# Performance work log

Measured on AMD Instinct MI355X. Metric: run time of the kernel, lower is better.

The kernel has to match this reference:

```python
import jax, jax.numpy as jnp
import numpy as np

B, S, H = 1, 2048, 2048
NH, NKV, HD = 16, 4, 128
E, K, I = 16, 4, 1024
ISH = 1024  # moe_intermediate_size * num_shared_experts
EPS = 1e-6
THETA = 10000.0


def setup_inputs():
    key = jax.random.key(0)
    ks = jax.random.split(key, 8)
    sd = 0.02
    return {
        "hidden_states": jax.random.normal(ks[0], (B, S, H), jnp.float32),
        "position_ids": jnp.broadcast_to(jnp.arange(S, dtype=jnp.int32), (B, S)),
        "ln1_w": jnp.ones((H,), jnp.float32),
        "ln2_w": jnp.ones((H,), jnp.float32),
        "w_qkv": jax.random.normal(ks[1], (H, (NH + 2 * NKV) * HD), jnp.float32) * sd,
        "w_o": jax.random.normal(ks[2], (NH * HD, H), jnp.float32) * sd,
        "w_gate": jax.random.normal(ks[3], (H, E), jnp.float32) * sd,
        "w_gu": jax.random.normal(ks[4], (E, H, 2 * I), jnp.float32) * sd,
        "w_down": jax.random.normal(ks[5], (E, I, H), jnp.float32) * sd,
        "w_sh_gu": jax.random.normal(ks[6], (H, 2 * ISH), jnp.float32) * sd,
        "w_sh_down": jax.random.normal(ks[7], (ISH, H), jnp.float32) * sd,
    }


def rmsnorm(x, w):
    xf = x.astype(jnp.float32)
    var = jnp.mean(xf * xf, axis=-1, keepdims=True)
    return (xf * jax.lax.rsqrt(var + EPS)).astype(x.dtype) * w


def apply_rope(x, pos):
    # x: [B, S, nh, HD]; neox style, rotary_dim == head_dim
    half = HD // 2
    inv_freq = 1.0 / (THETA ** (jnp.arange(0, HD, 2, dtype=jnp.float32) / HD))
    freqs = pos.astype(jnp.float32)[..., None] * inv_freq  # [B,S,half]
    cos = jnp.cos(freqs)[:, :, None, :]
    sin = jnp.sin(freqs)[:, :, None, :]
    x1, x2 = x[..., :half], x[..., half:]
    return jnp.concatenate([x1 * cos - x2 * sin, x1 * sin + x2 * cos], axis=-1)


def reference(hidden_states, position_ids, ln1_w, ln2_w, w_qkv, w_o, w_gate,
              w_gu, w_down, w_sh_gu, w_sh_down):
    # --- input RMSNorm (residual is None on entry) ---
    residual = hidden_states
    x = rmsnorm(hidden_states, ln1_w)

    # --- attention (GQA + neox RoPE, causal) ---
    qkv = x @ w_qkv
    q = qkv[..., : NH * HD].reshape(B, S, NH, HD)
    k = qkv[..., NH * HD:(NH + NKV) * HD].reshape(B, S, NKV, HD)
    v = qkv[..., (NH + NKV) * HD:].reshape(B, S, NKV, HD)
    q = apply_rope(q, position_ids)
    k = apply_rope(k, position_ids)
    rep = NH // NKV
    k = jnp.repeat(k, rep, axis=2)
    v = jnp.repeat(v, rep, axis=2)
    scores = jnp.einsum('bqhd,bkhd->bhqk', q, k) * (HD ** -0.5)
    causal = jnp.tril(jnp.ones((S, S), bool))
    scores = jnp.where(causal[None, None], scores, jnp.float32(-1e9))
    probs = jax.nn.softmax(scores, axis=-1)
    ctx = jnp.einsum('bhqk,bkhd->bqhd', probs, v).reshape(B, S, NH * HD)
    attn_out = ctx @ w_o

    # --- fused add + post-attention RMSNorm ---
    residual = residual + attn_out
    x = rmsnorm(residual, ln2_w)

    # --- MoE ---
    xt = x.reshape(-1, H)  # [T, H]
    logits = xt @ w_gate
    rprobs = jax.nn.softmax(logits, axis=-1)
    tw, ti = jax.lax.top_k(rprobs, K)  # [T,K]
    tw = tw / jnp.sum(tw, axis=-1, keepdims=True)  # norm_topk_prob=True
    combine = jnp.sum(jax.nn.one_hot(ti, E, dtype=tw.dtype) * tw[..., None], axis=1)  # [T,E]

    moe_out = jnp.zeros_like(xt)
    for e in range(E):  # fixed small expert count
        gu = xt @ w_gu[e]
        g, u = jnp.split(gu, 2, axis=-1)
        y = (jax.nn.silu(g) * u) @ w_down[e]
        moe_out = moe_out + combine[:, e:e + 1] * y

    # shared expert MLP
    gu = xt @ w_sh_gu
    g, u = jnp.split(gu, 2, axis=-1)
    moe_out = moe_out + (jax.nn.silu(g) * u) @ w_sh_down

    hidden = residual + moe_out.reshape(B, S, H)
    return hidden
```

## Files before the change

kernel.cpp:

```cpp
#include <hip/hip_runtime.h>
#include <hip/hip_bf16.h>
#include <math.h>

#define DI __device__ __forceinline__

typedef __attribute__((ext_vector_type(8))) short bf16x8;
typedef __attribute__((ext_vector_type(4))) short bf16x4;
typedef __attribute__((ext_vector_type(8))) _Float16 f16x8;
typedef __attribute__((ext_vector_type(4))) _Float16 f16x4;
typedef __attribute__((ext_vector_type(4))) float f32x4;

DI float b2f(short s) {
    unsigned u = ((unsigned)(unsigned short)s) << 16;
    return __builtin_bit_cast(float, u);
}
DI short f2b(float f) {
    unsigned u = __builtin_bit_cast(unsigned, f);
    unsigned r = (u + 0x7fffu + ((u >> 16) & 1u)) >> 16;
    return (short)(unsigned short)r;
}
struct hl16 { _Float16 h, l; };
DI hl16 fsp(float f) {
    hl16 r;
    r.h = (_Float16)f;
    r.l = (_Float16)((f - (float)r.h) * 2048.0f);
    return r;
}

template <int MODE>
__global__ __launch_bounds__(256) void rmsnorm_k(const float* __restrict__ x,
                                                 const float* __restrict__ w,
                                                 void* __restrict__ o1,
                                                 void* __restrict__ o2) {
    int row = blockIdx.x, tid = threadIdx.x;
    const float* xr = x + (long)row * 2048;
    float4 a = *(const float4*)(xr + tid * 8);
    float4 b = *(const float4*)(xr + tid * 8 + 4);
    float ss = a.x * a.x + a.y * a.y + a.z * a.z + a.w * a.w +
               b.x * b.x + b.y * b.y + b.z * b.z + b.w * b.w;
    for (int m = 1; m < 64; m <<= 1) ss += __shfl_xor(ss, m);
    __shared__ float red[4];
    if ((tid & 63) == 0) red[tid >> 6] = ss;
    __syncthreads();
    float sc = rsqrtf((red[0] + red[1] + red[2] + red[3]) * (1.0f / 2048.0f) + 1e-6f);
    float4 wa = *(const float4*)(w + tid * 8);
    float4 wb = *(const float4*)(w + tid * 8 + 4);
    float v[8] = {a.x * sc * wa.x, a.y * sc * wa.y, a.z * sc * wa.z, a.w * sc * wa.w,
                  b.x * sc * wb.x, b.y * sc * wb.y, b.z * sc * wb.z, b.w * sc * wb.w};
    if (MODE == 0) {
        f16x8 h, l;
        for (int j = 0; j < 8; ++j) { hl16 t = fsp(v[j]); h[j] = t.h; l[j] = t.l; }
        *(f16x8*)((_Float16*)o1 + (long)row * 2048 + tid * 8) = h;
        *(f16x8*)((_Float16*)o2 + (long)row * 2048 + tid * 8) = l;
    } else {
        bf16x8 o;
        for (int j = 0; j < 8; ++j) o[j] = f2b(v[j]);
        *(bf16x8*)((short*)o1 + (long)row * 2048 + tid * 8) = o;
    }
}

__global__ __launch_bounds__(256) void tsplit_k(const float* __restrict__ in, int ldin,
                                                _Float16* __restrict__ outh,
                                                _Float16* __restrict__ outl, int ldout) {
    __shared__ float t[64][68];
    int r0 = blockIdx.x * 64, c0 = blockIdx.y * 64;
    int tid = threadIdx.x;
    int rr = tid >> 2, cs = (tid & 3) * 16;
    const float* src = in + (long)(r0 + rr) * ldin + c0 + cs;
    for (int u = 0; u < 4; ++u) {
        float4 v = *(const float4*)(src + u * 4);
        t[rr][cs + u * 4 + 0] = v.x; t[rr][cs + u * 4 + 1] = v.y;
        t[rr][cs + u * 4 + 2] = v.z; t[rr][cs + u * 4 + 3] = v.w;
    }
    __syncthreads();
    int cr = tid >> 2, rs = (tid & 3) * 16;
    f16x8 h0, l0, h1, l1;
    for (int u = 0; u < 8; ++u)  { hl16 e = fsp(t[rs + u][cr]);     h0[u] = e.h; l0[u] = e.l; }
    for (int u = 0; u < 8; ++u)  { hl16 e = fsp(t[rs + 8 + u][cr]); h1[u] = e.h; l1[u] = e.l; }
    long ob = (long)(c0 + cr) * ldout + r0 + rs;
    *(f16x8*)(outh + ob) = h0; *(f16x8*)(outh + ob + 8) = h1;
    *(f16x8*)(outl + ob) = l0; *(f16x8*)(outl + ob + 8) = l1;
}

__global__ __launch_bounds__(256) void wprep_k(const float* __restrict__ in,
                                               short* __restrict__ outp,
                                               int R, int C) {
    __shared__ float t[64][68];
    int r0 = blockIdx.x * 64, c0 = blockIdx.y * 64;
    long es = (long)R * C;
    in += blockIdx.z * es;
    outp += blockIdx.z * es;
    int tid = threadIdx.x;
    int rr = tid >> 2, cs = (tid & 3) * 16;
    const float* src = in + (long)(r0 + rr) * C + c0 + cs;
    for (int u = 0; u < 4; ++u) {
        float4 v = *(const float4*)(src + u * 4);
        t[rr][cs + u * 4 + 0] = v.x; t[rr][cs + u * 4 + 1] = v.y;
        t[rr][cs + u * 4 + 2] = v.z; t[rr][cs + u * 4 + 3] = v.w;
    }
    __syncthreads();
    int cr = tid >> 2, rs = (tid & 3) * 16;
    bf16x8 o0, o1;
    for (int u = 0; u < 8; ++u) o0[u] = f2b(t[rs + u][cr]);
    for (int u = 0; u < 8; ++u) o1[u] = f2b(t[rs + 8 + u][cr]);
    long ob = (long)(c0 + cr) * R + r0 + rs;
    *(bf16x8*)(outp + ob) = o0;
    *(bf16x8*)(outp + ob + 8) = o1;
}

enum { EPI_F32 = 0, EPI_RESID = 1 };

template <int EPI>
__global__ __launch_bounds__(256) void pgemm_k(
    const _Float16* __restrict__ Ah, const _Float16* __restrict__ Al, int lda,
    const _Float16* __restrict__ Bh, const _Float16* __restrict__ Bl, int ldb,
    float* __restrict__ C, int ldc,
    const float* __restrict__ resid, int K) {
    __shared__ __align__(16) _Float16 sAh[128][72], sAl[128][72];
    __shared__ __align__(16) _Float16 sBh[64][72], sBl[64][72];
    int n0 = blockIdx.x * 64, m0 = blockIdx.y * 128;
    int tid = threadIdx.x, lane = tid & 63, wv = tid >> 6;
    int wm = (wv >> 1) * 64, wn = (wv & 1) * 32;
    int ln = lane & 15, g8 = (lane >> 4) * 8, rg = lane >> 4;
    int tr = tid >> 3, tc = (tid & 7) * 8;

    f32x4 a1[4][2], a2[4][2];
    for (int i = 0; i < 4; ++i)
        for (int j = 0; j < 2; ++j) { a1[i][j] = f32x4{0,0,0,0}; a2[i][j] = f32x4{0,0,0,0}; }

    for (int k0 = 0; k0 < K; k0 += 64) {
        for (int s = 0; s < 4; ++s) {
            int r = tr + s * 32;
            long ga = (long)(m0 + r) * lda + k0 + tc;
            *(f16x8*)&sAh[r][tc] = *(const f16x8*)(Ah + ga);
            *(f16x8*)&sAl[r][tc] = *(const f16x8*)(Al + ga);
        }
        for (int s = 0; s < 2; ++s) {
            int r = tr + s * 32;
            long gb = (long)(n0 + r) * ldb + k0 + tc;
            *(f16x8*)&sBh[r][tc] = *(const f16x8*)(Bh + gb);
            *(f16x8*)&sBl[r][tc] = *(const f16x8*)(Bl + gb);
        }
        __syncthreads();
        for (int kk = 0; kk < 2; ++kk) {
            f16x8 ah[4], alo[4], bh[2], blo[2];
            for (int i = 0; i < 4; ++i) {
                int r = wm + i * 16 + ln;
                ah[i]  = *(const f16x8*)&sAh[r][kk * 32 + g8];
                alo[i] = *(const f16x8*)&sAl[r][kk * 32 + g8];
            }
            for (int j = 0; j < 2; ++j) {
                int r = wn + j * 16 + ln;
                bh[j]  = *(const f16x8*)&sBh[r][kk * 32 + g8];
                blo[j] = *(const f16x8*)&sBl[r][kk * 32 + g8];
            }
            for (int i = 0; i < 4; ++i)
                for (int j = 0; j < 2; ++j) {
                    a1[i][j] = __builtin_amdgcn_mfma_f32_16x16x32_f16(ah[i], bh[j], a1[i][j], 0, 0, 0);
                    a2[i][j] = __builtin_amdgcn_mfma_f32_16x16x32_f16(alo[i], bh[j], a2[i][j], 0, 0, 0);
                    a2[i][j] = __builtin_amdgcn_mfma_f32_16x16x32_f16(ah[i], blo[j], a2[i][j], 0, 0, 0);
                }
        }
        __syncthreads();
    }
    for (int i = 0; i < 4; ++i)
        for (int r = 0; r < 4; ++r) {
            int m = m0 + wm + i * 16 + rg * 4 + r;
            for (int j = 0; j < 2; ++j) {
                int col = n0 + wn + j * 16 + ln;
                float v = a1[i][j][r] + a2[i][j][r] * (1.0f / 2048.0f);
                if (EPI == EPI_RESID) v += resid[(long)m * ldc + col];
                C[(long)m * ldc + col] = v;
            }
        }
}

enum { MEPI_BF16 = 0, MEPI_ATOMIC = 1 };

template <int EPI, bool EXPERT>
__global__ __launch_bounds__(256) void bgemm_k(
    const short* __restrict__ A, int lda,
    const short* __restrict__ Bt, int ldb, long bStride,
    void* __restrict__ C, int ldc,
    const int* __restrict__ perm, const float* __restrict__ permw,
    const int* __restrict__ offsets,
    int K, int gatherA, int gatherC) {
    __shared__ __align__(16) short sA[128][72], sB[128][72];

    int n0 = blockIdx.x * 128;
    int base = 0, cnt = 1 << 30, m0;
    if (EXPERT) {
        int e = blockIdx.y >> 4;
        m0 = (blockIdx.y & 15) * 128;
        base = offsets[e];
        cnt = offsets[e + 1] - base;
        if (m0 >= cnt) return;
        Bt += (long)e * bStride;
    } else {
        m0 = blockIdx.y * 128;
    }

    int tid = threadIdx.x, lane = tid & 63, wv = tid >> 6;
    int wm = (wv >> 1) * 64, wn = (wv & 1) * 64;
    int ln = lane & 15, g8 = (lane >> 4) * 8, rg = lane >> 4;
    int tr = tid >> 3, tc = (tid & 7) * 8;

    const short* aRow[4];
    for (int s = 0; s < 4; ++s) {
        int m = m0 + tr + s * 32;
        if (EXPERT && m >= cnt) m = cnt - 1;
        int arow;
        if (EXPERT) arow = gatherA ? perm[base + m] : (base + m);
        else arow = m;
        aRow[s] = A + (long)arow * lda;
    }

    f32x4 acc[4][4];
    for (int i = 0; i < 4; ++i)
        for (int j = 0; j < 4; ++j) acc[i][j] = f32x4{0.f, 0.f, 0.f, 0.f};

    for (int k0 = 0; k0 < K; k0 += 64) {
        for (int s = 0; s < 4; ++s) {
            int r = tr + s * 32;
            *(bf16x8*)&sA[r][tc] = *(const bf16x8*)(aRow[s] + k0 + tc);
            *(bf16x8*)&sB[r][tc] = *(const bf16x8*)(Bt + (long)(n0 + r) * ldb + k0 + tc);
        }
        __syncthreads();
        for (int kk = 0; kk < 2; ++kk) {
            bf16x8 af[4], bfr[4];
            for (int i = 0; i < 4; ++i)
                af[i] = *(const bf16x8*)&sA[wm + i * 16 + ln][kk * 32 + g8];
            for (int j = 0; j < 4; ++j)
                bfr[j] = *(const bf16x8*)&sB[wn + j * 16 + ln][kk * 32 + g8];
            for (int i = 0; i < 4; ++i)
                for (int j = 0; j < 4; ++j)
                    acc[i][j] = __builtin_amdgcn_mfma_f32_16x16x32_bf16(af[i], bfr[j], acc[i][j], 0, 0, 0);
        }
        __syncthreads();
    }

    for (int i = 0; i < 4; ++i) {
        for (int r = 0; r < 4; ++r) {
            int m = m0 + wm + i * 16 + rg * 4 + r;
            if (EXPERT && m >= cnt) continue;
            int crow;
            if (EXPERT) crow = gatherC ? perm[base + m] : (base + m);
            else crow = m;
            float cs = 1.0f;
            if (EPI == MEPI_ATOMIC && EXPERT && gatherC) cs = permw[base + m];
            for (int j = 0; j < 4; ++j) {
                int col = n0 + wn + j * 16 + ln;
                float v = acc[i][j][r];
                if (EPI == MEPI_BF16)
                    ((short*)C)[(long)crow * ldc + col] = f2b(v);
                else
                    atomicAdd(&((float*)C)[(long)crow * ldc + col], v * cs);
            }
        }
    }
}

__global__ __launch_bounds__(64) void ropetab_k(const int* __restrict__ pos,
                                                float* __restrict__ tab) {
    int s = blockIdx.x, d = threadIdx.x;
    double inv = pow(10000.0, -(double)d / 64.0);
    double fr = (double)pos[s] * inv;
    tab[s * 128 + d] = (float)cos(fr);
    tab[s * 128 + 64 + d] = (float)sin(fr);
}

__global__ __launch_bounds__(256) void ropeall_k(float* __restrict__ qkvf,
                                                 const float* __restrict__ tab,
                                                 _Float16* __restrict__ kh,
                                                 _Float16* __restrict__ kl) {
    int s = blockIdx.x, sub = threadIdx.x >> 6, d = threadIdx.x & 63;
    int hh = blockIdx.y * 4 + sub;
    float c = tab[s * 128 + d], sn = tab[s * 128 + 64 + d];
    if (hh < 16) {
        float* row = qkvf + (long)s * 3072 + hh * 128;
        float x1 = row[d], x2 = row[d + 64];
        row[d] = x1 * c - x2 * sn;
        row[d + 64] = x1 * sn + x2 * c;
    } else {
        int kvh = hh - 16;
        const float* row = qkvf + (long)s * 3072 + 2048 + kvh * 128;
        float x1 = row[d], x2 = row[d + 64];
        float y1 = x1 * c - x2 * sn, y2 = x1 * sn + x2 * c;
        hl16 a = fsp(y1), b = fsp(y2);
        long base = ((long)kvh * 2048 + s) * 128;
        kh[base + d] = a.h; kl[base + d] = a.l;
        kh[base + 64 + d] = b.h; kl[base + 64 + d] = b.l;
    }
}

__global__ __launch_bounds__(256) void vprep_k(const float* __restrict__ qkvf,
                                               _Float16* __restrict__ vth,
                                               _Float16* __restrict__ vtl) {
    __shared__ float t[64][68];
    int s0 = blockIdx.x * 64, d0 = blockIdx.y * 64, kvh = blockIdx.z;
    int tid = threadIdx.x;
    int rr = tid >> 2, cs = (tid & 3) * 16;
    const float* src = qkvf + (long)(s0 + rr) * 3072 + 2560 + kvh * 128 + d0 + cs;
    for (int u = 0; u < 4; ++u) {
        float4 v = *(const float4*)(src + u * 4);
        t[rr][cs + u * 4 + 0] = v.x; t[rr][cs + u * 4 + 1] = v.y;
        t[rr][cs + u * 4 + 2] = v.z; t[rr][cs + u * 4 + 3] = v.w;
    }
    __syncthreads();
    int dr = tid >> 2, ss = (tid & 3) * 16;
    f16x8 h0, l0, h1, l1;
    for (int u = 0; u < 8; ++u)  { hl16 e = fsp(t[ss + u][dr]);     h0[u] = e.h; l0[u] = e.l; }
    for (int u = 0; u < 8; ++u)  { hl16 e = fsp(t[ss + 8 + u][dr]); h1[u] = e.h; l1[u] = e.l; }
    long ob = ((long)kvh * 128 + d0 + dr) * 2048 + s0 + ss;
    *(f16x8*)(vth + ob) = h0; *(f16x8*)(vth + ob + 8) = h1;
    *(f16x8*)(vtl + ob) = l0; *(f16x8*)(vtl + ob + 8) = l1;
}

__global__ __launch_bounds__(256) void attn_k(
    const float* __restrict__ qkvf,
    const _Float16* __restrict__ kh, const _Float16* __restrict__ kl,
    const _Float16* __restrict__ vth, const _Float16* __restrict__ vtl,
    float* __restrict__ opart, float* __restrict__ mpart, float* __restrict__ lpart) {
    __shared__ __align__(16) _Float16 sKh[32][136], sKl[32][136];
    __shared__ __align__(16) _Float16 sVh[128][44], sVl[128][44];
    __shared__ __align__(16) _Float16 sPh[4][16][44], sPl[4][16][44];

    int bid = blockIdx.x, h = blockIdx.y, kvh = h >> 2;
    int qt = 0, cum = 0;
    for (int q = 0; q < 32; ++q) {
        int ch = (q >> 2) + 1;
        if (bid < cum + ch) { qt = q; break; }
        cum += ch;
    }
    int ci = bid - cum;
    int nt = 2 * (qt + 1);
    int t0 = ci * 8;
    int t1 = t0 + 8 < nt ? t0 + 8 : nt;
    int q0 = qt * 64;
    int tid = threadIdx.x, lane = tid & 63, wv = tid >> 6;
    int ln = lane & 15, g8 = (lane >> 4) * 8, rg = lane >> 4;

    f16x8 qh[4], ql[4];
    {
        int qrow = q0 + wv * 16 + ln;
        for (int ds = 0; ds < 4; ++ds) {
            const float* qp = qkvf + (long)qrow * 3072 + h * 128 + ds * 32 + g8;
            for (int j = 0; j < 8; ++j) { hl16 t = fsp(qp[j]); qh[ds][j] = t.h; ql[ds][j] = t.l; }
        }
    }

    f32x4 o[8];
    for (int i = 0; i < 8; ++i) o[i] = f32x4{0, 0, 0, 0};
    float mrow[4], lrow[4], al[4];
    for (int r = 0; r < 4; ++r) { mrow[r] = -3e38f; lrow[r] = 0.0f; }
    const float scale = 0.08838834764831845f;
    const float ILO = 1.0f / 2048.0f;

    int kr = tid >> 3, kc = (tid & 7) * 16;
    int vr = tid >> 1, vc = (tid & 1) * 16;

    for (int kt = t0; kt < t1; ++kt) {
        int kb = kt * 32;
        {
            long gb = ((long)kvh * 2048 + kb + kr) * 128 + kc;
            *(f16x8*)&sKh[kr][kc]     = *(const f16x8*)(kh + gb);
            *(f16x8*)&sKh[kr][kc + 8] = *(const f16x8*)(kh + gb + 8);
            *(f16x8*)&sKl[kr][kc]     = *(const f16x8*)(kl + gb);
            *(f16x8*)&sKl[kr][kc + 8] = *(const f16x8*)(kl + gb + 8);
        }
        {
            long gb = ((long)kvh * 128 + vr) * 2048 + kb + vc;
            *(f16x8*)&sVh[vr][vc]     = *(const f16x8*)(vth + gb);
            *(f16x8*)&sVh[vr][vc + 8] = *(const f16x8*)(vth + gb + 8);
            *(f16x8*)&sVl[vr][vc]     = *(const f16x8*)(vtl + gb);
            *(f16x8*)&sVl[vr][vc + 8] = *(const f16x8*)(vtl + gb + 8);
        }
        __syncthreads();

        f32x4 s1[2], s2[2];
        for (int j = 0; j < 2; ++j) { s1[j] = f32x4{0,0,0,0}; s2[j] = f32x4{0,0,0,0}; }
        for (int ds = 0; ds < 4; ++ds)
            for (int j = 0; j < 2; ++j) {
                int r = j * 16 + ln;
                f16x8 kfh = *(const f16x8*)&sKh[r][ds * 32 + g8];
                f16x8 kfl = *(const f16x8*)&sKl[r][ds * 32 + g8];
                s1[j] = __builtin_amdgcn_mfma_f32_16x16x32_f16(qh[ds], kfh, s1[j], 0, 0, 0);
                s2[j] = __builtin_amdgcn_mfma_f32_16x16x32_f16(ql[ds], kfh, s2[j], 0, 0, 0);
                s2[j] = __builtin_amdgcn_mfma_f32_16x16x32_f16(qh[ds], kfl, s2[j], 0, 0, 0);
            }

        float sv[2][4];
        bool dg = (kt >= 2 * qt);
        for (int j = 0; j < 2; ++j)
            for (int r = 0; r < 4; ++r) {
                float v = (s1[j][r] + s2[j][r] * ILO) * scale;
                if (dg) {
                    int col = kb + j * 16 + ln;
                    int rw = q0 + wv * 16 + rg * 4 + r;
                    if (col > rw) v = -1e9f;
                }
                sv[j][r] = v;
            }
        for (int r = 0; r < 4; ++r) {
            float mx = fmaxf(sv[0][r], sv[1][r]);
            for (int m = 1; m < 16; m <<= 1) mx = fmaxf(mx, __shfl_xor(mx, m));
            float mn = fmaxf(mrow[r], mx);
            al[r] = __expf(mrow[r] - mn);
            mrow[r] = mn;
            float rs = 0.0f;
            for (int j = 0; j < 2; ++j) {
                float p = __expf(sv[j][r] - mn);
                sv[j][r] = p;
                rs += p;
            }
            for (int m = 1; m < 16; m <<= 1) rs += __shfl_xor(rs, m);
            lrow[r] = lrow[r] * al[r] + rs;
        }
        for (int j = 0; j < 2; ++j)
            for (int r = 0; r < 4; ++r) {
                hl16 t = fsp(sv[j][r]);
                sPh[wv][rg * 4 + r][j * 16 + ln] = t.h;
                sPl[wv][rg * 4 + r][j * 16 + ln] = t.l;
            }
        for (int i = 0; i < 8; ++i)
            for (int r = 0; r < 4; ++r) o[i][r] *= al[r];
        f16x8 pah = *(const f16x8*)&sPh[wv][ln][g8];
        f16x8 pal = *(const f16x8*)&sPl[wv][ln][g8];
        f32x4 p2[8];
        for (int i = 0; i < 8; ++i) p2[i] = f32x4{0, 0, 0, 0};
        for (int i = 0; i < 8; ++i) {
            f16x8 vfh = *(const f16x8*)&sVh[i * 16 + ln][g8];
            f16x8 vfl = *(const f16x8*)&sVl[i * 16 + ln][g8];
            o[i]  = __builtin_amdgcn_mfma_f32_16x16x32_f16(pah, vfh, o[i], 0, 0, 0);
            p2[i] = __builtin_amdgcn_mfma_f32_16x16x32_f16(pal, vfh, p2[i], 0, 0, 0);
            p2[i] = __builtin_amdgcn_mfma_f32_16x16x32_f16(pah, vfl, p2[i], 0, 0, 0);
        }
        for (int i = 0; i < 8; ++i)
            for (int r = 0; r < 4; ++r) o[i][r] += p2[i][r] * ILO;
        __syncthreads();
    }

    long idx = (long)h * 144 + bid;
    float* ob = opart + idx * 8192;
    for (int r = 0; r < 4; ++r) {
        int rl = wv * 16 + rg * 4 + r;
        if (ln == 0) { mpart[idx * 64 + rl] = mrow[r]; lpart[idx * 64 + rl] = lrow[r]; }
        for (int i = 0; i < 8; ++i)
            ob[rl * 128 + i * 16 + ln] = o[i][r];
    }
}

__global__ __launch_bounds__(256) void merge_k(const float* __restrict__ opart,
                                               const float* __restrict__ mpart,
                                               const float* __restrict__ lpart,
                                               _Float16* __restrict__ ctxh,
                                               _Float16* __restrict__ ctxl) {
    int qt = blockIdx.x, h = blockIdx.y;
    int nch = (qt >> 2) + 1;
    int cum = 0;
    for (int q = 0; q < qt; ++q) cum += (q >> 2) + 1;
    long base = (long)h * 144 + cum;
    int tid = threadIdx.x;
    int cg = (tid & 15) * 8;
    for (int pass = 0; pass < 4; ++pass) {
        int row = pass * 16 + (tid >> 4);
        float mv[8], a[8];
        float M = -3e38f;
#pragma unroll
        for (int c = 0; c < 8; ++c) {
            mv[c] = (c < nch) ? mpart[(base + c) * 64 + row] : -3e38f;
            M = fmaxf(M, mv[c]);
        }
        float L = 0.f;
#pragma unroll
        for (int c = 0; c < 8; ++c) {
            a[c] = (c < nch) ? __expf(mv[c] - M) : 0.f;
            if (c < nch) L += lpart[(base + c) * 64 + row] * a[c];
        }
        float inv = 1.0f / L;
        float acc[8];
#pragma unroll
        for (int j = 0; j < 8; ++j) acc[j] = 0.f;
#pragma unroll
        for (int c = 0; c < 8; ++c) {
            if (c < nch) {
                const float* p = opart + (base + c) * 8192 + row * 128 + cg;
                float4 v0 = *(const float4*)(p);
                float4 v1 = *(const float4*)(p + 4);
                acc[0] += v0.x * a[c]; acc[1] += v0.y * a[c];
                acc[2] += v0.z * a[c]; acc[3] += v0.w * a[c];
                acc[4] += v1.x * a[c]; acc[5] += v1.y * a[c];
                acc[6] += v1.z * a[c]; acc[7] += v1.w * a[c];
            }
        }
        f16x8 oh, ol;
#pragma unroll
        for (int j = 0; j < 8; ++j) {
            hl16 t = fsp(acc[j] * inv);
            oh[j] = t.h; ol[j] = t.l;
        }
        long grow = (long)(qt * 64 + row) * 2048 + h * 128 + cg;
        *(f16x8*)(ctxh + grow) = oh;
        *(f16x8*)(ctxl + grow) = ol;
    }
}

__global__ __launch_bounds__(256) void router_k(const float* __restrict__ res,
                                                const float* __restrict__ w2,
                                                const float* __restrict__ wg,
                                                int* __restrict__ ti, float* __restrict__ tw) {
    int t = blockIdx.x, tid = threadIdx.x;
    const float* xr = res + (long)t * 2048;
    float4 a = *(const float4*)(xr + tid * 8);
    float4 b = *(const float4*)(xr + tid * 8 + 4);
    float ss = a.x * a.x + a.y * a.y + a.z * a.z + a.w * a.w +
               b.x * b.x + b.y * b.y + b.z * b.z + b.w * b.w;
    for (int m = 1; m < 64; m <<= 1) ss += __shfl_xor(ss, m);
    __shared__ float red[4];
    __shared__ float lg[4][16];
    if ((tid & 63) == 0) red[tid >> 6] = ss;
    __syncthreads();
    float sc = rsqrtf((red[0] + red[1] + red[2] + red[3]) * (1.0f / 2048.0f) + 1e-6f);
    float part[16];
    for (int e = 0; e < 16; ++e) part[e] = 0.f;
    for (int k = tid; k < 2048; k += 256) {
        float xv = xr[k] * sc * w2[k];
        const float* wr = wg + k * 16;
        for (int e = 0; e < 16; ++e) part[e] += xv * wr[e];
    }
    for (int e = 0; e < 16; ++e)
        for (int m = 1; m < 64; m <<= 1) part[e] += __shfl_xor(part[e], m);
    if ((tid & 63) == 0)
        for (int e = 0; e < 16; ++e) lg[tid >> 6][e] = part[e];
    __syncthreads();
    if (tid == 0) {
        float logit[16];
        float mx = -3e38f;
        for (int e = 0; e < 16; ++e) {
            logit[e] = lg[0][e] + lg[1][e] + lg[2][e] + lg[3][e];
            mx = fmaxf(mx, logit[e]);
        }
        float sum = 0.f, pr[16];
        for (int e = 0; e < 16; ++e) { pr[e] = expf(logit[e] - mx); sum += pr[e]; }
        for (int e = 0; e < 16; ++e) pr[e] /= sum;
        int sel[4]; float sw[4]; float s4 = 0.f;
        unsigned used = 0;
        for (int j = 0; j < 4; ++j) {
            int be = 0; float bv = -1.f;
            for (int e = 0; e < 16; ++e)
                if (!((used >> e) & 1u) && pr[e] > bv) { bv = pr[e]; be = e; }
            used |= 1u << be; sel[j] = be; sw[j] = bv; s4 += bv;
        }
        for (int j = 0; j < 4; ++j) {
            ti[t * 4 + j] = sel[j];
            tw[t * 4 + j] = sw[j] / s4;
        }
    }
}

__global__ void build1_k(const int* __restrict__ ti, int* __restrict__ offs, int* __restrict__ curs) {
    __shared__ int c[16];
    int tid = threadIdx.x;
    if (tid < 16) c[tid] = 0;
    __syncthreads();
    for (int i = tid; i < 8192; i += 256) atomicAdd(&c[ti[i]], 1);
    __syncthreads();
    if (tid == 0) {
        int run = 0;
        for (int e = 0; e < 16; ++e) { offs[e] = run; curs[e] = run; run += c[e]; }
        offs[16] = run;
    }
}

__global__ void build2_k(const int* __restrict__ ti, const float* __restrict__ tw,
                         int* __restrict__ curs, int* __restrict__ perm, float* __restrict__ permw) {
    int i = blockIdx.x * 256 + threadIdx.x;
    if (i < 8192) {
        int e = ti[i];
        int pos = atomicAdd(&curs[e], 1);
        perm[pos] = i >> 2;
        permw[pos] = tw[i];
    }
}

__global__ __launch_bounds__(256) void silu_k(const short* __restrict__ gu,
                                              short* __restrict__ act, int total) {
    int idx = blockIdx.x * 256 + threadIdx.x;
    if (idx >= total) return;
    int row = idx >> 7, c8 = (idx & 127) * 8;
    bf16x8 g = *(const bf16x8*)(gu + (long)row * 2048 + c8);
    bf16x8 u = *(const bf16x8*)(gu + (long)row * 2048 + 1024 + c8);
    bf16x8 o;
    for (int j = 0; j < 8; ++j) {
        float gf = b2f(g[j]), uf = b2f(u[j]);
        float s = gf / (1.0f + __expf(-gf));
        o[j] = f2b(s * uf);
    }
    *(bf16x8*)(act + (long)row * 1024 + c8) = o;
}

extern "C" void kernel_launch(void* const* d_in, const int* in_sizes, int n_in,
                              void* d_out, int out_size, void* d_ws, size_t ws_size,
                              hipStream_t stream) {
    const float* hidden    = (const float*)d_in[0];
    const int*   posids    = (const int*)d_in[1];
    const float* ln1       = (const float*)d_in[2];
    const float* ln2       = (const float*)d_in[3];
    const float* w_qkv     = (const float*)d_in[4];
    const float* w_o       = (const float*)d_in[5];
    const float* w_gate    = (const float*)d_in[6];
    const float* w_gu      = (const float*)d_in[7];
    const float* w_down    = (const float*)d_in[8];
    const float* w_sh_gu   = (const float*)d_in[9];
    const float* w_sh_down = (const float*)d_in[10];
    float* out = (float*)d_out;

    char* ws = (char*)d_ws;
    _Float16* xh    = (_Float16*)(ws + 0);
    _Float16* xl    = (_Float16*)(ws + 8388608);
    float*    qkvf  = (float*)   (ws + 16777216);
    _Float16* kh    = (_Float16*)(ws + 41943040);
    _Float16* kl    = (_Float16*)(ws + 44040192);
    _Float16* vth   = (_Float16*)(ws + 46137344);
    _Float16* vtl   = (_Float16*)(ws + 48234496);
    _Float16* ctxh  = (_Float16*)(ws + 50331648);
    _Float16* ctxl  = (_Float16*)(ws + 58720256);
    _Float16* wTh   = (_Float16*)(ws + 67108864);
    _Float16* wTl   = (_Float16*)(ws + 79691776);
    _Float16* woTh  = (_Float16*)(ws + 67108864);
    _Float16* woTl  = (_Float16*)(ws + 75497472);
    float*    opart = (float*)   (ws + 92274688);
    float*    mpart = (float*)   (ws + 167772160);
    float*    lpart = (float*)   (ws + 168361984);
    float*    rtab  = (float*)   (ws + 168951808);
    short*    x2b      = (short*)(ws + 0);
    short*    w_guT    = (short*)(ws + 8388608);
    short*    gu       = (short*)(ws + 142606336);
    short*    act      = (short*)(ws + 8388608);
    short*    w_downT  = (short*)(ws + 25165824);
    short*    w_shguT  = (short*)(ws + 92274688);
    short*    shgu     = (short*)(ws + 100663296);
    short*    shact    = (short*)(ws + 109051904);
    short*    w_shdownT= (short*)(ws + 113246208);
    char*     rb       = ws + 176160768;
    int*   topk_idx = (int*)(rb);
    float* topk_w   = (float*)(rb + 32 * 1024);
    int*   perm     = (int*)(rb + 64 * 1024);
    float* permw    = (float*)(rb + 96 * 1024);
    int*   offs     = (int*)(rb + 128 * 1024);
    int*   curs     = (int*)(rb + 128 * 1024 + 256);

    ropetab_k<<<2048, 64, 0, stream>>>(posids, rtab);
    rmsnorm_k<0><<<2048, 256, 0, stream>>>(hidden, ln1, xh, xl);
    tsplit_k<<<dim3(32, 48), 256, 0, stream>>>(w_qkv, 3072, wTh, wTl, 2048);
    pgemm_k<EPI_F32><<<dim3(48, 16), 256, 0, stream>>>(xh, xl, 2048, wTh, wTl, 2048,
                                                       qkvf, 3072, nullptr, 2048);
    ropeall_k<<<dim3(2048, 5), 256, 0, stream>>>(qkvf, rtab, kh, kl);
    vprep_k<<<dim3(32, 2, 4), 256, 0, stream>>>(qkvf, vth, vtl);
    attn_k<<<dim3(144, 16), 256, 0, stream>>>(qkvf, kh, kl, vth, vtl,
                                              opart, mpart, lpart);
    merge_k<<<dim3(32, 16), 256, 0, stream>>>(opart, mpart, lpart, ctxh, ctxl);
    tsplit_k<<<dim3(32, 32), 256, 0, stream>>>(w_o, 2048, woTh, woTl, 2048);
    pgemm_k<EPI_RESID><<<dim3(32, 16), 256, 0, stream>>>(ctxh, ctxl, 2048, woTh, woTl, 2048,
                                                         out, 2048, hidden, 2048);
    rmsnorm_k<1><<<2048, 256, 0, stream>>>(out, ln2, x2b, nullptr);
    router_k<<<2048, 256, 0, stream>>>(out, ln2, w_gate, topk_idx, topk_w);
    build1_k<<<1, 256, 0, stream>>>(topk_idx, offs, curs);
    build2_k<<<32, 256, 0, stream>>>(topk_idx, topk_w, curs, perm, permw);
    wprep_k<<<dim3(32, 32, 16), 256, 0, stream>>>(w_gu, w_guT, 2048, 2048);
    bgemm_k<MEPI_BF16, true><<<dim3(16, 256), 256, 0, stream>>>(
        x2b, 2048, w_guT, 2048, (long)2048 * 2048, gu, 2048, perm, permw, offs, 2048, 1, 0);
    silu_k<<<4096, 256, 0, stream>>>(gu, act, 8192 * 128);
    wprep_k<<<dim3(16, 32, 16), 256, 0, stream>>>(w_down, w_downT, 1024, 2048);
    bgemm_k<MEPI_ATOMIC, true><<<dim3(16, 256), 256, 0, stream>>>(
        act, 1024, w_downT, 1024, (long)1024 * 2048, out, 2048, perm, permw, offs, 1024, 0, 1);
    wprep_k<<<dim3(32, 32, 1), 256, 0, stream>>>(w_sh_gu, w_shguT, 2048, 2048);
    bgemm_k<MEPI_BF16, false><<<dim3(16, 16), 256, 0, stream>>>(
        x2b, 2048, w_shguT, 2048, 0, shgu, 2048, perm, permw, offs, 2048, 0, 0);
    silu_k<<<1024, 256, 0, stream>>>(shgu, shact, 2048 * 128);
    wprep_k<<<dim3(16, 32, 1), 256, 0, stream>>>(w_sh_down, w_shdownT, 1024, 2048);
    bgemm_k<MEPI_ATOMIC, false><<<dim3(16, 16), 256, 0, stream>>>(
        shact, 1024, w_shdownT, 1024, 0, out, 2048, perm, permw, offs, 1024, 0, 0);
}
```

Before: 828.1 us.

## Double attention query tile per block to reuse K/V shared-memory loads

Each attention block now handles 128 query rows instead of 64, with every wave processing two 16-row groups so the K and V tiles loaded into shared memory feed twice as many MFMAs. The split-KV chunking, the partial-output layout and the merge kernel are rescaled to match (72 blocks per head, 128-row partials). This halves K/V global traffic and syncs per unit of work, but doubles accumulator registers per thread (occupancy risk) and leaves fewer blocks to spread across the GPU.

```diff
diff --git a/kernel.cpp b/kernel.cpp
--- a/kernel.cpp
+++ b/kernel.cpp
@@ -323,36 +323,38 @@
     float* __restrict__ opart, float* __restrict__ mpart, float* __restrict__ lpart) {
     __shared__ __align__(16) _Float16 sKh[32][136], sKl[32][136];
     __shared__ __align__(16) _Float16 sVh[128][44], sVl[128][44];
-    __shared__ __align__(16) _Float16 sPh[4][16][44], sPl[4][16][44];
+    __shared__ __align__(16) _Float16 sPh[4][32][44], sPl[4][32][44];
 
     int bid = blockIdx.x, h = blockIdx.y, kvh = h >> 2;
-    int qt = 0, cum = 0;
-    for (int q = 0; q < 32; ++q) {
-        int ch = (q >> 2) + 1;
-        if (bid < cum + ch) { qt = q; break; }
+    int Q = 0, cum = 0;
+    for (int q = 0; q < 16; ++q) {
+        int ch = (q + 2) >> 1;
+        if (bid < cum + ch) { Q = q; break; }
         cum += ch;
     }
     int ci = bid - cum;
-    int nt = 2 * (qt + 1);
+    int nt = 4 * Q + 4;
     int t0 = ci * 8;
-    int t1 = t0 + 8 < nt ? t0 + 8 : nt;
-    int q0 = qt * 64;
+    int t1 = (t0 + 8 < nt) ? t0 + 8 : nt;
+    int q0 = Q * 128;
     int tid = threadIdx.x, lane = tid & 63, wv = tid >> 6;
     int ln = lane & 15, g8 = (lane >> 4) * 8, rg = lane >> 4;
 
-    f16x8 qh[4], ql[4];
-    {
-        int qrow = q0 + wv * 16 + ln;
+    f16x8 qh[2][4], ql[2][4];
+    for (int g = 0; g < 2; ++g) {
+        int qrow = q0 + wv * 32 + g * 16 + ln;
         for (int ds = 0; ds < 4; ++ds) {
             const float* qp = qkvf + (long)qrow * 3072 + h * 128 + ds * 32 + g8;
-            for (int j = 0; j < 8; ++j) { hl16 t = fsp(qp[j]); qh[ds][j] = t.h; ql[ds][j] = t.l; }
-        }
-    }
-
-    f32x4 o[8];
-    for (int i = 0; i < 8; ++i) o[i] = f32x4{0, 0, 0, 0};
-    float mrow[4], lrow[4], al[4];
-    for (int r = 0; r < 4; ++r) { mrow[r] = -3e38f; lrow[r] = 0.0f; }
+            for (int j = 0; j < 8; ++j) { hl16 t = fsp(qp[j]); qh[g][ds][j] = t.h; ql[g][ds][j] = t.l; }
+        }
+    }
+
+    f32x4 o[2][8];
+    for (int g = 0; g < 2; ++g)
+        for (int i = 0; i < 8; ++i) o[g][i] = f32x4{0, 0, 0, 0};
+    float mrow[2][4], lrow[2][4];
+    for (int g = 0; g < 2; ++g)
+        for (int r = 0; r < 4; ++r) { mrow[g][r] = -3e38f; lrow[g][r] = 0.0f; }
     const float scale = 0.08838834764831845f;
     const float ILO = 1.0f / 2048.0f;
 
@@ -377,77 +379,87 @@
         }
         __syncthreads();
 
-        f32x4 s1[2], s2[2];
-        for (int j = 0; j < 2; ++j) { s1[j] = f32x4{0,0,0,0}; s2[j] = f32x4{0,0,0,0}; }
+        f32x4 s1[2][2], s2[2][2];
+        for (int g = 0; g < 2; ++g)
+            for (int j = 0; j < 2; ++j) { s1[g][j] = f32x4{0,0,0,0}; s2[g][j] = f32x4{0,0,0,0}; }
         for (int ds = 0; ds < 4; ++ds)
             for (int j = 0; j < 2; ++j) {
                 int r = j * 16 + ln;
                 f16x8 kfh = *(const f16x8*)&sKh[r][ds * 32 + g8];
                 f16x8 kfl = *(const f16x8*)&sKl[r][ds * 32 + g8];
-                s1[j] = __builtin_amdgcn_mfma_f32_16x16x32_f16(qh[ds], kfh, s1[j], 0, 0, 0);
-                s2[j] = __builtin_amdgcn_mfma_f32_16x16x32_f16(ql[ds], kfh, s2[j], 0, 0, 0);
-                s2[j] = __builtin_amdgcn_mfma_f32_16x16x32_f16(qh[ds], kfl, s2[j], 0, 0, 0);
-            }
-
-        float sv[2][4];
-        bool dg = (kt >= 2 * qt);
-        for (int j = 0; j < 2; ++j)
+                for (int g = 0; g < 2; ++g) {
+                    s1[g][j] = __builtin_amdgcn_mfma_f32_16x16x32_f16(qh[g][ds], kfh, s1[g][j], 0, 0, 0);
+                    s2[g][j] = __builtin_amdgcn_mfma_f32_16x16x32_f16(ql[g][ds], kfh, s2[g][j], 0, 0, 0);
+                    s2[g][j] = __builtin_amdgcn_mfma_f32_16x16x32_f16(qh[g][ds], kfl, s2[g][j], 0, 0, 0);
+                }
+            }
+
+        for (int g = 0; g < 2; ++g) {
+            int rowbase = q0 + wv * 32 + g * 16;
+            bool dg = (kb + 31 > rowbase);
+            float sv[2][4];
+            for (int j = 0; j < 2; ++j)
+                for (int r = 0; r < 4; ++r) {
+                    float v = (s1[g][j][r] + s2[g][j][r] * ILO) * scale;
+                    if (dg) {
+                        int col = kb + j * 16 + ln;
+                        int rw = rowbase + rg * 4 + r;
+                        if (col > rw) v = -1e9f;
+                    }
+                    sv[j][r] = v;
+                }
             for (int r = 0; r < 4; ++r) {
-                float v = (s1[j][r] + s2[j][r] * ILO) * scale;
-                if (dg) {
-                    int col = kb + j * 16 + ln;
-                    int rw = q0 + wv * 16 + rg * 4 + r;
-                    if (col > rw) v = -1e9f;
+                float mx = fmaxf(sv[0][r], sv[1][r]);
+                for (int m = 1; m < 16; m <<= 1) mx = fmaxf(mx, __shfl_xor(mx, m));
+                float mn = fmaxf(mrow[g][r], mx);
+                float alv = __expf(mrow[g][r] - mn);
+                mrow[g][r] = mn;
+                float rs = 0.0f;
+                for (int j = 0; j < 2; ++j) {
+                    float p = __expf(sv[j][r] - mn);
+                    sv[j][r] = p;
+                    rs += p;
                 }
-                sv[j][r] = v;
-            }
-        for (int r = 0; r < 4; ++r) {
-            float mx = fmaxf(sv[0][r], sv[1][r]);
-            for (int m = 1; m < 16; m <<= 1) mx = fmaxf(mx, __shfl_xor(mx, m));
-            float mn = fmaxf(mrow[r], mx);
-            al[r] = __expf(mrow[r] - mn);
-            mrow[r] = mn;
-            float rs = 0.0f;
-            for (int j = 0; j < 2; ++j) {
-                float p = __expf(sv[j][r] - mn);
-                sv[j][r] = p;
-                rs += p;
-            }
-            for (int m = 1; m < 16; m <<= 1) rs += __shfl_xor(rs, m);
-            lrow[r] = lrow[r] * al[r] + rs;
-        }
-        for (int j = 0; j < 2; ++j)
-            for (int r = 0; r < 4; ++r) {
-                hl16 t = fsp(sv[j][r]);
-                sPh[wv][rg * 4 + r][j * 16 + ln] = t.h;
-                sPl[wv][rg * 4 + r][j * 16 + ln] = t.l;
-            }
-        for (int i = 0; i < 8; ++i)
-            for (int r = 0; r < 4; ++r) o[i][r] *= al[r];
-        f16x8 pah = *(const f16x8*)&sPh[wv][ln][g8];
-        f16x8 pal = *(const f16x8*)&sPl[wv][ln][g8];
-        f32x4 p2[8];
-        for (int i = 0; i < 8; ++i) p2[i] = f32x4{0, 0, 0, 0};
+                for (int m = 1; m < 16; m <<= 1) rs += __shfl_xor(rs, m);
+                lrow[g][r] = lrow[g][r] * alv + rs;
+                for (int i = 0; i < 8; ++i) o[g][i][r] *= alv;
+            }
+            for (int j = 0; j < 2; ++j)
+                for (int r = 0; r < 4; ++r) {
+                    hl16 t = fsp(sv[j][r]);
+                    sPh[wv][g * 16 + rg * 4 + r][j * 16 + ln] = t.h;
+                    sPl[wv][g * 16 + rg * 4 + r][j * 16 + ln] = t.l;
+                }
+        }
+
+        f16x8 pah[2], pal[2];
+        for (int g = 0; g < 2; ++g) {
+            pah[g] = *(const f16x8*)&sPh[wv][g * 16 + ln][g8];
+            pal[g] = *(const f16x8*)&sPl[wv][g * 16 + ln][g8];
+        }
         for (int i = 0; i < 8; ++i) {
             f16x8 vfh = *(const f16x8*)&sVh[i * 16 + ln][g8];
             f16x8 vfl = *(const f16x8*)&sVl[i * 16 + ln][g8];
-            o[i]  = __builtin_amdgcn_mfma_f32_16x16x32_f16(pah, vfh, o[i], 0, 0, 0);
-            p2[i] = __builtin_amdgcn_mfma_f32_16x16x32_f16(pal, vfh, p2[i], 0, 0, 0);
-            p2[i] = __builtin_amdgcn_mfma_f32_16x16x32_f16(pah, vfl, p2[i], 0, 0, 0);
-        }
-        for (int i = 0; i < 8; ++i)
-            for (int r = 0; r < 4; ++r) o[i][r] += p2[i][r] * ILO;
+            for (int g = 0; g < 2; ++g) {
+                o[g][i] = __builtin_amdgcn_mfma_f32_16x16x32_f16(pah[g], vfh, o[g][i], 0, 0, 0);
+                f32x4 t = f32x4{0, 0, 0, 0};
+                t = __builtin_amdgcn_mfma_f32_16x16x32_f16(pal[g], vfh, t, 0, 0, 0);
+                t = __builtin_amdgcn_mfma_f32_16x16x32_f16(pah[g], vfl, t, 0, 0, 0);
+                for (int r = 0; r < 4; ++r) o[g][i][r] += t[r] * ILO;
+            }
+        }
         __syncthreads();
     }
 
-    long idx = (long)h * 144 + bid;
-    float* ob = opart + idx * 8192;
-    for (int r = 0; r < 4; ++r) {
-        int rl = wv * 16 + rg * 4 + r;
-        if (ln == 0) { mpart[idx * 64 + rl] = mrow[r]; lpart[idx * 64 + rl] = lrow[r]; }
-        for (int i = 0; i < 8; ++i)
-            ob[rl * 128 + i * 16 + ln] = o[i][r];
-    }
+    long idx = (long)h * 72 + bid;
+    float* ob = opart + idx * 16384;
+    for (int g = 0; g < 2; ++g)
+        for (int r = 0; r < 4; ++r) {
+            int rl = wv * 32 + g * 16 + rg * 4 + r;
+            if (ln == 0) { mpart[idx * 128 + rl] = mrow[g][r]; lpart[idx * 128 + rl] = lrow[g][r]; }
+            for (int i = 0; i < 8; ++i)
+                ob[rl * 128 + i * 16 + ln] = o[g][i][r];
+        }
 }
 
 __global__ __launch_bounds__(256) void merge_k(const float* __restrict__ opart,
@@ -455,27 +467,27 @@
                                                const float* __restrict__ lpart,
                                                _Float16* __restrict__ ctxh,
                                                _Float16* __restrict__ ctxl) {
-    int qt = blockIdx.x, h = blockIdx.y;
-    int nch = (qt >> 2) + 1;
+    int Q = blockIdx.x, h = blockIdx.y;
+    int nch = (Q + 2) >> 1;
     int cum = 0;
-    for (int q = 0; q < qt; ++q) cum += (q >> 2) + 1;
-    long base = (long)h * 144 + cum;
+    for (int q = 0; q < Q; ++q) cum += (q + 2) >> 1;
+    long base = (long)h * 72 + cum;
     int tid = threadIdx.x;
     int cg = (tid & 15) * 8;
-    for (int pass = 0; pass < 4; ++pass) {
+    for (int pass = 0; pass < 8; ++pass) {
         int row = pass * 16 + (tid >> 4);
         float mv[8], a[8];
         float M = -3e38f;
 #pragma unroll
         for (int c = 0; c < 8; ++c) {
-            mv[c] = (c < nch) ? mpart[(base + c) * 64 + row] : -3e38f;
+            mv[c] = (c < nch) ? mpart[(base + c) * 128 + row] : -3e38f;
             M = fmaxf(M, mv[c]);
         }
         float L = 0.f;
 #pragma unroll
         for (int c = 0; c < 8; ++c) {
             a[c] = (c < nch) ? __expf(mv[c] - M) : 0.f;
-            if (c < nch) L += lpart[(base + c) * 64 + row] * a[c];
+            if (c < nch) L += lpart[(base + c) * 128 + row] * a[c];
         }
         float inv = 1.0f / L;
         float acc[8];
@@ -484,7 +496,7 @@
 #pragma unroll
         for (int c = 0; c < 8; ++c) {
             if (c < nch) {
-                const float* p = opart + (base + c) * 8192 + row * 128 + cg;
+                const float* p = opart + (base + c) * 16384 + row * 128 + cg;
                 float4 v0 = *(const float4*)(p);
                 float4 v1 = *(const float4*)(p + 4);
                 acc[0] += v0.x * a[c]; acc[1] += v0.y * a[c];
@@ -499,7 +511,7 @@
             hl16 t = fsp(acc[j] * inv);
             oh[j] = t.h; ol[j] = t.l;
         }
-        long grow = (long)(qt * 64 + row) * 2048 + h * 128 + cg;
+        long grow = (long)(Q * 128 + row) * 2048 + h * 128 + cg;
         *(f16x8*)(ctxh + grow) = oh;
         *(f16x8*)(ctxl + grow) = ol;
     }
@@ -657,9 +669,9 @@
                                                        qkvf, 3072, nullptr, 2048);
     ropeall_k<<<dim3(2048, 5), 256, 0, stream>>>(qkvf, rtab, kh, kl);
     vprep_k<<<dim3(32, 2, 4), 256, 0, stream>>>(qkvf, vth, vtl);
-    attn_k<<<dim3(144, 16), 256, 0, stream>>>(qkvf, kh, kl, vth, vtl,
-                                              opart, mpart, lpart);
-    merge_k<<<dim3(32, 16), 256, 0, stream>>>(opart, mpart, lpart, ctxh, ctxl);
+    attn_k<<<dim3(72, 16), 256, 0, stream>>>(qkvf, kh, kl, vth, vtl,
+                                             opart, mpart, lpart);
+    merge_k<<<dim3(16, 16), 256, 0, stream>>>(opart, mpart, lpart, ctxh, ctxl);
     tsplit_k<<<dim3(32, 32), 256, 0, stream>>>(w_o, 2048, woTh, woTl, 2048);
     pgemm_k<EPI_RESID><<<dim3(32, 16), 256, 0, stream>>>(ctxh, ctxl, 2048, woTh, woTl, 2048,
                                                          out, 2048, hidden, 2048);
```

Measured after the change: 952.7 us. 1.15x slower.
